# Performance work log

Hardware: AMD Instinct MI355X
Metric: run time of the kernel (lower is better)

## Reference

```python
import jax, jax.numpy as jnp
import numpy as np

B = 1_048_576
W = 64  # hidden width
N_FREQ = 6   # 3 dims * 6 freqs * (sin,cos) = 36
K_BLOB = 4   # one-blob bins per dim


def _freq_embed(p):
    # [B,3] -> [B,36]
    freqs = 2.0 ** jnp.arange(N_FREQ, dtype=p.dtype)
    ang = jnp.pi * p[:, :, None] * freqs  # [B,3,6]
    return jnp.concatenate([jnp.sin(ang), jnp.cos(ang)], axis=-1).reshape(p.shape[0], 3 * 2 * N_FREQ)


def _sph(d):
    # unit-square parameterization of a direction, [B,3] -> [B,2]
    d = d / (jnp.linalg.norm(d, axis=-1, keepdims=True) + 1e-8)
    u = jnp.arctan2(d[:, 1], d[:, 0]) / (2.0 * jnp.pi) + 0.5
    v = jnp.arccos(jnp.clip(d[:, 2], -1.0 + 1e-6, 1.0 - 1e-6)) / jnp.pi
    return jnp.stack([u, v], axis=-1)


def _one_blob(x, k=K_BLOB):
    # x in [0,1], [B,D] -> [B,D*k] Gaussian one-blob encoding
    centers = (jnp.arange(k, dtype=x.dtype) + 0.5) / k
    sigma = 1.0 / k
    g = jnp.exp(-0.5 * ((x[..., None] - centers) / sigma) ** 2)  # [B,D,k]
    return g.reshape(x.shape[0], -1)


def _encode(p, wi, n, alpha, beta, r):
    ones = jnp.ones((p.shape[0], 2), dtype=p.dtype)
    return jnp.concatenate([
        _freq_embed(p),                      # 36
        _one_blob(_sph(wi)),                 # 8
        _one_blob(_sph(n)),                  # 8
        _one_blob(1.0 - jnp.exp(-r)),        # 4
        alpha, beta,                         # 6
        ones,                                # 2 (implicit bias)
    ], axis=-1)                              # -> [B,64]


def _mlp(x, Ws):
    h = x
    for Wk in Ws[:-1]:
        h = jax.nn.relu(h @ Wk.T)
    return h @ Ws[-1].T  # [B,3]


def setup_inputs() -> dict:
    key = jax.random.key(0)
    ks = jax.random.split(key, 13)
    p = jax.random.normal(ks[0], (B, 3), jnp.float32)
    wi = jax.random.normal(ks[1], (B, 3), jnp.float32)
    n = jax.random.normal(ks[2], (B, 3), jnp.float32)
    alpha = jax.random.uniform(ks[3], (B, 3), jnp.float32)
    beta = jax.random.uniform(ks[4], (B, 3), jnp.float32)
    r = jax.random.uniform(ks[5], (B, 1), jnp.float32)
    s = 1.0 / np.sqrt(W)
    weights = {}
    for i in range(6):
        weights[f"W{i}"] = jax.random.normal(ks[6 + i], (W, W), jnp.float32) * s
    weights["W6"] = jax.random.normal(ks[12], (3, W), jnp.float32) * s
    return dict(p=p, wi=wi, n=n, alpha=alpha, beta=beta, r=r, **weights)


def reference(p, wi, n, alpha, beta, r, W0, W1, W2, W3, W4, W5, W6):
    x = _encode(p, wi, n, alpha, beta, r)
    out = _mlp(x, [W0, W1, W2, W3, W4, W5, W6])
    return out * (alpha + beta)  # reflectance factorization
```

## Files before the change

kernel.cpp:

```cpp
#include <hip/hip_runtime.h>


typedef _Float16 f16;
typedef f16 f16x2 __attribute__((ext_vector_type(2)));
typedef f16 f16x4 __attribute__((ext_vector_type(4)));
typedef f16 f16x8 __attribute__((ext_vector_type(8)));
typedef float f32x4 __attribute__((ext_vector_type(4)));

#define MFMA32(A, B, C) __builtin_amdgcn_mfma_f32_16x16x32_f16(A, B, C, 0, 0, 0)
#define LDS_FENCE() __asm__ volatile("" ::: "memory")

static constexpr int TILES = 4;
static constexpr int WAVES = 2;
static constexpr int BLOCK = WAVES * 64;
static constexpr int SPB   = WAVES * 64;

static constexpr int    WUNITS   = 50;
static constexpr size_t WS_BYTES = (size_t)WUNITS * 64 * 16;

__host__ __device__ __forceinline__ int tau(int x) {
    return (x & 32) + ((x & 7) >> 2) * 16 + ((x >> 3) & 3) * 4 + (x & 3);
}

__device__ __forceinline__ f16x2 pkh(float a, float b) {
    return __builtin_bit_cast(f16x2, __builtin_amdgcn_cvt_pkrtz(a, b));
}

__device__ __forceinline__ f16x8 pack8(const float* f) {
    f16x2 a = pkh(f[0], f[1]);
    f16x2 b = pkh(f[2], f[3]);
    f16x2 c = pkh(f[4], f[5]);
    f16x2 d = pkh(f[6], f[7]);
    f16x8 v;
    v[0] = a[0]; v[1] = a[1]; v[2] = b[0]; v[3] = b[1];
    v[4] = c[0]; v[5] = c[1]; v[6] = d[0]; v[7] = d[1];
    return v;
}

__device__ __forceinline__ f16x4 pack4(f32x4 v) {
    f16x2 a = pkh(v[0], v[1]);
    f16x2 b = pkh(v[2], v[3]);
    f16x4 r;
    r[0] = a[0]; r[1] = a[1]; r[2] = b[0]; r[3] = b[1];
    return r;
}

__device__ __forceinline__ float fast_atan2_rev(float y, float x) {
    const float ax = __builtin_fabsf(x), ay = __builtin_fabsf(y);
    const float mx = fmaxf(ax, ay), mn = fminf(ax, ay);
    const float a = mn * __builtin_amdgcn_rcpf(fmaxf(mx, 1e-30f));
    const float s = a * a;
    float r = a * (0.99997726f + s * (-0.33262347f + s * (0.19354346f +
              s * (-0.11643287f + s * (0.05265332f - s * 0.01172120f)))));
    if (ay > ax) r = 1.5707963268f - r;
    if (x < 0.0f) r = 3.1415926536f - r;
    r = (y < 0.0f) ? -r : r;
    return r * 0.15915494309189535f;
}

__device__ __forceinline__ float fast_acos(float x) {
    const float ax = __builtin_fabsf(x);
    const float t = __builtin_amdgcn_sqrtf(1.0f - ax);
    const float p = t * (1.5707288f + ax * (-0.2121144f +
                    ax * (0.0742610f - ax * 0.0187293f)));
    return (x < 0.0f) ? (3.1415926536f - p) : p;
}

__device__ __forceinline__ void blob4(float x, float* out) {
    const float dx = x - 0.125f;
    const float E0 = __expf(-8.0f * dx * dx);
    const float R  = __expf(4.0f * dx);
    const float t1 = R * 0.60653066f;
    const float t2 = R * 0.22313016f;
    const float t3 = R * 0.082084999f;
    out[0] = E0;
    out[1] = E0 * t1;
    out[2] = out[1] * t2;
    out[3] = out[2] * t3;
}

__global__ __launch_bounds__(256, 1) void pack_weights_kernel(
    const float* __restrict__ W0, const float* __restrict__ W1,
    const float* __restrict__ W2, const float* __restrict__ W3,
    const float* __restrict__ W4, const float* __restrict__ W5,
    const float* __restrict__ W6, f16* __restrict__ ws)
{
    const int u = (int)blockIdx.x * 256 + threadIdx.x;
    if (u >= WUNITS * 64) return;
    const int lane = u & 63;
    const int unit = u >> 6;
    const int q = lane >> 4, m = lane & 15;
    f16x8 v;
    if (unit < 48) {
        const int l = unit >> 3, kt = (unit & 7) >> 2, mt = unit & 3;
        const float* Ws[6] = {W0, W1, W2, W3, W4, W5};
        const float* __restrict__ Wl = Ws[l];
#pragma unroll
        for (int j = 0; j < 8; ++j) {
            const int x = kt * 32 + q * 8 + j;
            const int src = (l == 0) ? x : tau(x);
            v[j] = (f16)Wl[(mt * 16 + m) * 64 + src];
        }
    } else {
        const int kt = unit - 48;
#pragma unroll
        for (int j = 0; j < 8; ++j) {
            const int src = tau(kt * 32 + q * 8 + j);
            v[j] = (m < 3) ? (f16)W6[m * 64 + src] : (f16)0.0f;
        }
    }
    *(f16x8*)(ws + unit * 512 + lane * 8) = v;
}

__device__ __forceinline__ f16x8 cat44(f16x4 a, f16x4 b) {
    return __builtin_shufflevector(a, b, 0, 1, 2, 3, 4, 5, 6, 7);
}

template<int PACKED>
__global__ __launch_bounds__(BLOCK, 2) void nrc_mlp_kernel(
    const float* __restrict__ P,  const float* __restrict__ WI,
    const float* __restrict__ NV, const float* __restrict__ AL,
    const float* __restrict__ BE, const float* __restrict__ RR,
    const f16*   __restrict__ ws,
    const float* __restrict__ W0, const float* __restrict__ W1,
    const float* __restrict__ W2, const float* __restrict__ W3,
    const float* __restrict__ W4, const float* __restrict__ W5,
    const float* __restrict__ W6, float* __restrict__ Out)
{
    __shared__ __attribute__((aligned(16))) unsigned char smem[WAVES * 4096];

    const int tid  = threadIdx.x;
    const int lane = tid & 63;
    const int w    = tid >> 6;
    const int q    = lane >> 4;
    const int m    = lane & 15;
    unsigned char* const hb = smem + w * 4096;

    const int wave_base = (int)blockIdx.x * SPB + w * 64;

    float feat[64];
    float ab0, ab1, ab2;

    {
        const int s = wave_base + lane;

        float pv[3], wv[3], nv[3], av[3], bv[3];
#pragma unroll
        for (int d = 0; d < 3; ++d) {
            pv[d] = P [s * 3 + d];
            wv[d] = WI[s * 3 + d];
            nv[d] = NV[s * 3 + d];
            av[d] = AL[s * 3 + d];
            bv[d] = BE[s * 3 + d];
        }
        const float rv = RR[s];

#pragma unroll
        for (int d = 0; d < 3; ++d) {
            const float fr = __builtin_amdgcn_fractf(pv[d] * 0.5f);
            float sv = __builtin_amdgcn_sinf(fr);
            float cv = __builtin_amdgcn_cosf(fr);
            feat[d * 12 + 0] = sv;
            feat[d * 12 + 6] = cv;
#pragma unroll
            for (int k = 1; k < 6; ++k) {
                const float s2 = sv * sv;
                const float sc = sv * cv;
                cv = fmaf(-2.0f, s2, 1.0f);
                sv = sc + sc;
                feat[d * 12 + k]     = sv;
                feat[d * 12 + 6 + k] = cv;
            }
        }
#pragma unroll
        for (int which = 0; which < 2; ++which) {
            const float* dv = (which == 0) ? wv : nv;
            const int fo = 36 + which * 8;
            const float nr = __builtin_amdgcn_sqrtf(dv[0]*dv[0] + dv[1]*dv[1] + dv[2]*dv[2]) + 1e-8f;
            const float u  = fast_atan2_rev(dv[1], dv[0]) + 0.5f;
            float zc = dv[2] * __builtin_amdgcn_rcpf(nr);
            zc = fminf(fmaxf(zc, -1.0f + 1e-6f), 1.0f - 1e-6f);
            const float vv = fast_acos(zc) * 0.3183098861837907f;
            blob4(u,  &feat[fo]);
            blob4(vv, &feat[fo + 4]);
        }
        blob4(1.0f - __expf(-rv), &feat[52]);

        feat[56] = av[0]; feat[57] = av[1]; feat[58] = av[2];
        feat[59] = bv[0]; feat[60] = bv[1]; feat[61] = bv[2];
        feat[62] = 1.0f;  feat[63] = 1.0f;

        ab0 = av[0] + bv[0];
        ab1 = av[1] + bv[1];
        ab2 = av[2] + bv[2];
    }

    const int te = lane >> 4;
    f16x8 bf[TILES][2];
#pragma unroll
    for (int pass = 0; pass < 2; ++pass) {
        if ((te >> 1) == pass) {
            unsigned char* const tb = hb + (te & 1) * 2048 + m * 128;
#pragma unroll
            for (int g = 0; g < 8; ++g) {
                const int slot0 = (4 * g + 4 * m) & 31;
                *(f16x8*)(tb + slot0 * 4) = pack8(&feat[g * 8]);
            }
        }
        LDS_FENCE();
#pragma unroll
        for (int th = 0; th < 2; ++th) {
            const int t = pass * 2 + th;
#pragma unroll
            for (int kt = 0; kt < 2; ++kt) {
                const int s0 = (16 * kt + 4 * q + 4 * m) & 31;
                bf[t][kt] = *(const f16x8*)(hb + th * 2048 + m * 128 + s0 * 4);
            }
        }
        LDS_FENCE();
    }

    const f16* const wbase = ws + (size_t)lane * 8;
    const float* const Ws[6] = {W0, W1, W2, W3, W4, W5};
    const f16x4 zero4 = {(f16)0.0f, (f16)0.0f, (f16)0.0f, (f16)0.0f};

#pragma unroll
    for (int layer = 0; layer < 6; ++layer) {
        f16x8 wa[8];
        if (PACKED) {
#pragma unroll
            for (int f = 0; f < 8; ++f)
                wa[f] = *(const f16x8*)(wbase + (layer * 8 + f) * 512);
        } else {
            const float* __restrict__ Wl = Ws[layer];
#pragma unroll
            for (int kt = 0; kt < 2; ++kt)
#pragma unroll
                for (int mt = 0; mt < 4; ++mt) {
                    float tv[8];
#pragma unroll
                    for (int j = 0; j < 8; ++j) {
                        const int x = kt * 32 + q * 8 + j;
                        tv[j] = Wl[(mt * 16 + m) * 64 + (layer == 0 ? x : tau(x))];
                    }
                    wa[kt * 4 + mt] = pack8(tv);
                }
        }

#pragma unroll
        for (int t = 0; t < TILES; ++t) {
            f32x4 acc[4];
#pragma unroll
            for (int mt = 0; mt < 4; ++mt) {
                f32x4 z = {0.0f, 0.0f, 0.0f, 0.0f};
                z = MFMA32(wa[mt],     bf[t][0], z);
                z = MFMA32(wa[4 + mt], bf[t][1], z);
                acc[mt] = z;
            }
            f16x4 pk[4];
#pragma unroll
            for (int mt = 0; mt < 4; ++mt)
                pk[mt] = __builtin_elementwise_max(pack4(acc[mt]), zero4);
            bf[t][0] = cat44(pk[0], pk[1]);
            bf[t][1] = cat44(pk[2], pk[3]);
        }
    }

    {
        f16x8 w6f[2];
        if (PACKED) {
            w6f[0] = *(const f16x8*)(wbase + 48 * 512);
            w6f[1] = *(const f16x8*)(wbase + 49 * 512);
        } else {
#pragma unroll
            for (int kt = 0; kt < 2; ++kt) {
                float tv[8];
#pragma unroll
                for (int j = 0; j < 8; ++j) {
                    const int src = tau(kt * 32 + q * 8 + j);
                    tv[j] = (m < 3) ? W6[m * 64 + src] : 0.0f;
                }
                w6f[kt] = pack8(tv);
            }
        }
#pragma unroll
        for (int t = 0; t < TILES; ++t) {
            f32x4 z = {0.0f, 0.0f, 0.0f, 0.0f};
            z = MFMA32(w6f[0], bf[t][0], z);
            z = MFMA32(w6f[1], bf[t][1], z);
            const int src = t * 16 + m;
            const float s0 = __shfl(ab0, src);
            const float s1 = __shfl(ab1, src);
            const float s2 = __shfl(ab2, src);
            if (lane < 16) {
                const int s = wave_base + t * 16 + m;
                float* o = Out + s * 3;
                o[0] = z[0] * s0;
                o[1] = z[1] * s1;
                o[2] = z[2] * s2;
            }
        }
    }
}

extern "C" void kernel_launch(void* const* d_in, const int* in_sizes, int n_in,
                              void* d_out, int out_size, void* d_ws, size_t ws_size,
                              hipStream_t stream) {
    (void)n_in; (void)out_size;
    const float* P  = (const float*)d_in[0];
    const float* WI = (const float*)d_in[1];
    const float* NV = (const float*)d_in[2];
    const float* AL = (const float*)d_in[3];
    const float* BE = (const float*)d_in[4];
    const float* RR = (const float*)d_in[5];
    const float* W0 = (const float*)d_in[6];
    const float* W1 = (const float*)d_in[7];
    const float* W2 = (const float*)d_in[8];
    const float* W3 = (const float*)d_in[9];
    const float* W4 = (const float*)d_in[10];
    const float* W5 = (const float*)d_in[11];
    const float* W6 = (const float*)d_in[12];
    f16*   ws  = (f16*)d_ws;
    float* Out = (float*)d_out;

    const int Bn = in_sizes[0] / 3;
    const int grid = Bn / SPB;

    if (ws_size >= WS_BYTES) {
        hipLaunchKernelGGL(pack_weights_kernel, dim3((WUNITS * 64 + 255) / 256),
                           dim3(256), 0, stream, W0, W1, W2, W3, W4, W5, W6, ws);
        hipLaunchKernelGGL((nrc_mlp_kernel<1>), dim3(grid), dim3(BLOCK), 0, stream,
                           P, WI, NV, AL, BE, RR, ws,
                           W0, W1, W2, W3, W4, W5, W6, Out);
    } else {
        hipLaunchKernelGGL((nrc_mlp_kernel<0>), dim3(grid), dim3(BLOCK), 0, stream,
                           P, WI, NV, AL, BE, RR, ws,
                           W0, W1, W2, W3, W4, W5, W6, Out);
    }
}
```

Before: 159.3 us.

## Stage packed MLP weights in LDS per block and use four waves

Each block cooperatively copies all packed fp16 weight fragments into shared memory once, and every layer's MFMA operands are then read from LDS instead of global memory. Block size doubles to four waves, and the per-wave activation transpose buffer is halved, handling one tile per pass. This aims to cut repeated global/L2 weight traffic, but adds a 51 KB copy per block plus a barrier, and the larger LDS footprint may limit occupancy.

Measured after the change: 166.7 us. 4.7% more time.

```diff
diff --git a/kernel.cpp b/kernel.cpp
--- a/kernel.cpp
+++ b/kernel.cpp
@@ -11,12 +11,14 @@
 #define LDS_FENCE() __asm__ volatile("" ::: "memory")
 
 static constexpr int TILES = 4;
-static constexpr int WAVES = 2;
+static constexpr int WAVES = 4;
 static constexpr int BLOCK = WAVES * 64;
 static constexpr int SPB   = WAVES * 64;
 
 static constexpr int    WUNITS   = 50;
-static constexpr size_t WS_BYTES = (size_t)WUNITS * 64 * 16;
+static constexpr int    WCHUNKS  = WUNITS * 64;
+static constexpr size_t WS_BYTES = (size_t)WCHUNKS * 16;
+static constexpr int    LDS_W    = 51200;
 
 __host__ __device__ __forceinline__ int tau(int x) {
     return (x & 32) + ((x & 7) >> 2) * 16 + ((x >> 3) & 3) * 4 + (x & 3);
@@ -79,37 +81,46 @@
     out[3] = out[2] * t3;
 }
 
+__device__ __forceinline__ f16x8 make_wchunk(
+    int c, const float* __restrict__ W0, const float* __restrict__ W1,
+    const float* __restrict__ W2, const float* __restrict__ W3,
+    const float* __restrict__ W4, const float* __restrict__ W5,
+    const float* __restrict__ W6)
+{
+    const int lane2 = c & 63;
+    const int unit  = c >> 6;
+    const int q = lane2 >> 4, m = lane2 & 15;
+    f16x8 v;
+    if (unit < 48) {
+        const int l = unit >> 3, kt = (unit & 7) >> 2, mt = unit & 3;
+        const float* Ws[6] = {W0, W1, W2, W3, W4, W5};
+        const float* __restrict__ Wl = Ws[l];
+#pragma unroll
+        for (int j = 0; j < 8; ++j) {
+            const int x = kt * 32 + q * 8 + j;
+            const int src = (l == 0) ? x : tau(x);
+            v[j] = (f16)Wl[(mt * 16 + m) * 64 + src];
+        }
+    } else {
+        const int kt = unit - 48;
+#pragma unroll
+        for (int j = 0; j < 8; ++j) {
+            const int src = tau(kt * 32 + q * 8 + j);
+            v[j] = (m < 3) ? (f16)W6[m * 64 + src] : (f16)0.0f;
+        }
+    }
+    return v;
+}
+
 __global__ __launch_bounds__(256, 1) void pack_weights_kernel(
     const float* __restrict__ W0, const float* __restrict__ W1,
     const float* __restrict__ W2, const float* __restrict__ W3,
     const float* __restrict__ W4, const float* __restrict__ W5,
     const float* __restrict__ W6, f16* __restrict__ ws)
 {
-    const int u = (int)blockIdx.x * 256 + threadIdx.x;
-    if (u >= WUNITS * 64) return;
-    const int lane = u & 63;
-    const int unit = u >> 6;
-    const int q = lane >> 4, m = lane & 15;
-    f16x8 v;
-    if (unit < 48) {
-        const int l = unit >> 3, kt = (unit & 7) >> 2, mt = unit & 3;
-        const float* Ws[6] = {W0, W1, W2, W3, W4, W5};
-        const float* __restrict__ Wl = Ws[l];
-#pragma unroll
-        for (int j = 0; j < 8; ++j) {
-            const int x = kt * 32 + q * 8 + j;
-            const int src = (l == 0) ? x : tau(x);
-            v[j] = (f16)Wl[(mt * 16 + m) * 64 + src];
-        }
-    } else {
-        const int kt = unit - 48;
-#pragma unroll
-        for (int j = 0; j < 8; ++j) {
-            const int src = tau(kt * 32 + q * 8 + j);
-            v[j] = (m < 3) ? (f16)W6[m * 64 + src] : (f16)0.0f;
-        }
-    }
-    *(f16x8*)(ws + unit * 512 + lane * 8) = v;
+    const int c = (int)blockIdx.x * 256 + threadIdx.x;
+    if (c >= WCHUNKS) return;
+    *(f16x8*)(ws + (size_t)c * 8) = make_wchunk(c, W0, W1, W2, W3, W4, W5, W6);
 }
 
 __device__ __forceinline__ f16x8 cat44(f16x4 a, f16x4 b) {
@@ -127,16 +138,28 @@
     const float* __restrict__ W4, const float* __restrict__ W5,
     const float* __restrict__ W6, float* __restrict__ Out)
 {
-    __shared__ __attribute__((aligned(16))) unsigned char smem[WAVES * 4096];
+    __shared__ __attribute__((aligned(16))) unsigned char smem[LDS_W + WAVES * 2048];
 
     const int tid  = threadIdx.x;
     const int lane = tid & 63;
     const int w    = tid >> 6;
     const int q    = lane >> 4;
     const int m    = lane & 15;
-    unsigned char* const hb = smem + w * 4096;
+    unsigned char* const wlds = smem;
+    unsigned char* const hb   = smem + LDS_W + w * 2048;
 
     const int wave_base = (int)blockIdx.x * SPB + w * 64;
+
+#pragma unroll
+    for (int i = 0; i < (WCHUNKS + BLOCK - 1) / BLOCK; ++i) {
+        const int c = i * BLOCK + tid;
+        if (c < WCHUNKS) {
+            f16x8 v;
+            if (PACKED) v = *(const f16x8*)(ws + (size_t)c * 8);
+            else        v = make_wchunk(c, W0, W1, W2, W3, W4, W5, W6);
+            *(f16x8*)(wlds + c * 16) = v;
+        }
+    }
 
     float feat[64];
     float ab0, ab1, ab2;
@@ -198,9 +221,9 @@
     const int te = lane >> 4;
     f16x8 bf[TILES][2];
 #pragma unroll
-    for (int pass = 0; pass < 2; ++pass) {
-        if ((te >> 1) == pass) {
-            unsigned char* const tb = hb + (te & 1) * 2048 + m * 128;
+    for (int pass = 0; pass < TILES; ++pass) {
+        if (te == pass) {
+            unsigned char* const tb = hb + m * 128;
 #pragma unroll
             for (int g = 0; g < 8; ++g) {
                 const int slot0 = (4 * g + 4 * m) & 31;
@@ -209,43 +232,24 @@
         }
         LDS_FENCE();
 #pragma unroll
-        for (int th = 0; th < 2; ++th) {
-            const int t = pass * 2 + th;
-#pragma unroll
-            for (int kt = 0; kt < 2; ++kt) {
-                const int s0 = (16 * kt + 4 * q + 4 * m) & 31;
-                bf[t][kt] = *(const f16x8*)(hb + th * 2048 + m * 128 + s0 * 4);
-            }
+        for (int kt = 0; kt < 2; ++kt) {
+            const int s0 = (16 * kt + 4 * q + 4 * m) & 31;
+            bf[pass][kt] = *(const f16x8*)(hb + m * 128 + s0 * 4);
         }
         LDS_FENCE();
     }
 
-    const f16* const wbase = ws + (size_t)lane * 8;
-    const float* const Ws[6] = {W0, W1, W2, W3, W4, W5};
+    __syncthreads();
+
     const f16x4 zero4 = {(f16)0.0f, (f16)0.0f, (f16)0.0f, (f16)0.0f};
+    unsigned char* const wb = wlds + lane * 16;
 
 #pragma unroll
     for (int layer = 0; layer < 6; ++layer) {
         f16x8 wa[8];
-        if (PACKED) {
-#pragma unroll
-            for (int f = 0; f < 8; ++f)
-                wa[f] = *(const f16x8*)(wbase + (layer * 8 + f) * 512);
-        } else {
-            const float* __restrict__ Wl = Ws[layer];
-#pragma unroll
-            for (int kt = 0; kt < 2; ++kt)
-#pragma unroll
-                for (int mt = 0; mt < 4; ++mt) {
-                    float tv[8];
-#pragma unroll
-                    for (int j = 0; j < 8; ++j) {
-                        const int x = kt * 32 + q * 8 + j;
-                        tv[j] = Wl[(mt * 16 + m) * 64 + (layer == 0 ? x : tau(x))];
-                    }
-                    wa[kt * 4 + mt] = pack8(tv);
-                }
-        }
+#pragma unroll
+        for (int f = 0; f < 8; ++f)
+            wa[f] = *(const f16x8*)(wb + (layer * 8 + f) * 1024);
 
 #pragma unroll
         for (int t = 0; t < TILES; ++t) {
@@ -267,27 +271,13 @@
     }
 
     {
-        f16x8 w6f[2];
-        if (PACKED) {
-            w6f[0] = *(const f16x8*)(wbase + 48 * 512);
-            w6f[1] = *(const f16x8*)(wbase + 49 * 512);
-        } else {
-#pragma unroll
-            for (int kt = 0; kt < 2; ++kt) {
-                float tv[8];
-#pragma unroll
-                for (int j = 0; j < 8; ++j) {
-                    const int src = tau(kt * 32 + q * 8 + j);
-                    tv[j] = (m < 3) ? W6[m * 64 + src] : 0.0f;
-                }
-                w6f[kt] = pack8(tv);
-            }
-        }
+        const f16x8 w6f0 = *(const f16x8*)(wb + 48 * 1024);
+        const f16x8 w6f1 = *(const f16x8*)(wb + 49 * 1024);
 #pragma unroll
         for (int t = 0; t < TILES; ++t) {
             f32x4 z = {0.0f, 0.0f, 0.0f, 0.0f};
-            z = MFMA32(w6f[0], bf[t][0], z);
-            z = MFMA32(w6f[1], bf[t][1], z);
+            z = MFMA32(w6f0, bf[t][0], z);
+            z = MFMA32(w6f1, bf[t][1], z);
             const int src = t * 16 + m;
             const float s0 = __shfl(ab0, src);
             const float s1 = __shfl(ab1, src);
@@ -327,7 +317,7 @@
     const int grid = Bn / SPB;
 
     if (ws_size >= WS_BYTES) {
-        hipLaunchKernelGGL(pack_weights_kernel, dim3((WUNITS * 64 + 255) / 256),
+        hipLaunchKernelGGL(pack_weights_kernel, dim3((WCHUNKS + 255) / 256),
                            dim3(256), 0, stream, W0, W1, W2, W3, W4, W5, W6, ws);
         hipLaunchKernelGGL((nrc_mlp_kernel<1>), dim3(grid), dim3(BLOCK), 0, stream,
                            P, WI, NV, AL, BE, RR, ws,
```
